# Kernel tuning notes

Hardware: AMD Instinct MI355X
Metric: run time of the kernel (lower is better)

Reference implementation:

```python
import jax, jax.numpy as jnp
import numpy as np

T, B, I, H, O = 2048, 128, 32, 128, 1


def setup_inputs() -> dict:
    key = jax.random.key(0)
    ks = jax.random.split(key, 5)
    X = jax.random.normal(ks[0], (T, B, I), dtype=jnp.float32)
    W_in = jax.random.normal(ks[1], (H, I), dtype=jnp.float32) / np.sqrt(I)
    W_hh = jax.random.normal(ks[2], (H, H), dtype=jnp.float32) / np.sqrt(H)
    rnn_bias = jnp.zeros((H,), dtype=jnp.float32)
    alpha = jax.random.uniform(ks[3], (H,), dtype=jnp.float32)
    value_W = jax.random.normal(ks[4], (O, H), dtype=jnp.float32) / np.sqrt(H)
    value_bias = jnp.zeros((O,), dtype=jnp.float32)
    return {"X": X, "W_in": W_in, "W_hh": W_hh, "rnn_bias": rnn_bias,
            "alpha": alpha, "value_W": value_W, "value_bias": value_bias}


def reference(X, W_in, W_hh, rnn_bias, alpha, value_W, value_bias):
    # X: (T, B, I). Precompute input projections for all timesteps at once.
    xproj = jnp.einsum('tbi,hi->tbh', X, W_in)  # (T, B, H)

    def step(h_prev, xp_t):
        h_tilde = jnp.tanh(xp_t + h_prev @ W_hh.T + rnn_bias)
        h = (1.0 - alpha) * h_prev + alpha * h_tilde  # per-unit leaky blend
        return h, h

    h0 = jnp.zeros((X.shape[1], W_hh.shape[0]), dtype=X.dtype)
    last_hidden, Z = jax.lax.scan(step, h0, xproj)  # Z: (T, B, H)
    V = value_bias + jnp.einsum('tbh,oh->tbo', Z, value_W)  # (T, B, O)
    return V, last_hidden
```

## Files before the change

kernel.cpp:

```cpp
#include <hip/hip_runtime.h>

#define TT 2048
#define BB 128
#define II 32
#define HH 128

typedef float v2f __attribute__((ext_vector_type(2)));
typedef float v4f __attribute__((ext_vector_type(4)));

__device__ __forceinline__ v2f pk_fma(v2f a, v2f b, v2f c) {
    v2f d;
    asm("v_pk_fma_f32 %0, %1, %2, %3" : "=v"(d) : "v"(a), "v"(b), "v"(c));
    return d;
}

template <int CTRL>
__device__ __forceinline__ float dpp_add(float p) {
    int t = __builtin_amdgcn_update_dpp(0, __float_as_int(p), CTRL, 0xF, 0xF, true);
    return p + __int_as_float(t);
}

__global__ __launch_bounds__(512)
void vrnn_kernel(const float* __restrict__ X, const float* __restrict__ W_in,
                 const float* __restrict__ W_hh, const float* __restrict__ rnn_bias,
                 const float* __restrict__ alpha, const float* __restrict__ value_W,
                 const float* __restrict__ value_bias, float* __restrict__ out)
{
    const int b    = blockIdx.x;
    const int tid  = threadIdx.x;
    const int wave = tid >> 6;
    const int lane = tid & 63;
    const int g    = lane >> 4;
    const int j    = lane & 15;
    const int base = 16 * wave + 4 * g;

    __shared__ __align__(16) float hbuf[2 * HH];
    __shared__ __align__(16) float xs[2 * 288];
    __shared__ __align__(16) float vpart[2][8];

    v2f wh[4][4], wi[4], binit[4];
#pragma unroll
    for (int r = 0; r < 4; ++r) {
        const float* wr = W_hh + (size_t)(base + r) * HH + 8 * j;
        v4f a0 = *reinterpret_cast<const v4f*>(wr);
        v4f a1 = *reinterpret_cast<const v4f*>(wr + 4);
        wh[r][0] = (v2f){a0.x, a0.y}; wh[r][1] = (v2f){a0.z, a0.w};
        wh[r][2] = (v2f){a1.x, a1.y}; wh[r][3] = (v2f){a1.z, a1.w};
        wi[r] = *reinterpret_cast<const v2f*>(W_in + (size_t)(base + r) * II + 2 * j);
        binit[r] = (v2f){ (j == 0) ? rnn_bias[base + r] : 0.0f, 0.0f };
    }
    const bool j1 = (j & 1) != 0;
    const bool j2 = (j & 2) != 0;
    const float al     = alpha[base + (j & 3)];
    const float vw_eff = (j < 4) ? value_W[base + j] : 0.0f;
    const float vb     = value_bias[0];

    if (tid < HH) hbuf[tid] = 0.0f;

    const int xr = lane >> 3;
    const int xc = (lane & 7) * 4;
    v4f xpend;
    if (wave == 0) {
        v4f w0 = *reinterpret_cast<const v4f*>(X + (size_t)xr * (BB * II) + b * II + xc);
        xpend  = *reinterpret_cast<const v4f*>(X + (size_t)(8 + xr) * (BB * II) + b * II + xc);
        *reinterpret_cast<v4f*>(&xs[xr * 36 + xc]) = w0;
    }
    float hval = 0.0f;
    __syncthreads();

    float* outV = out;
    float* outH = out + (size_t)TT * BB;

    for (int t2 = 0; t2 < TT / 16; ++t2) {
#pragma unroll
        for (int s = 0; s < 16; ++s) {
            if ((s & 7) == 0 && wave == 0) {
                *reinterpret_cast<v4f*>(&xs[(((s >> 3) + 1) & 1) * 288 + xr * 36 + xc]) = xpend;
                int row = (t2 << 4) + ((s >> 3) << 3) + 16 + xr;
                if (row > TT - 1) row = TT - 1;
                xpend = *reinterpret_cast<const v4f*>(X + (size_t)row * (BB * II) + b * II + xc);
            }
            if ((s != 0 || t2 != 0) && tid == 0) {
                const float* vp = vpart[(s & 1) ^ 1];
                float sum = vb;
#pragma unroll
                for (int w = 0; w < 8; ++w) sum += vp[w];
                const int t = (t2 << 4) + s;
                outV[(size_t)(t - 1) * BB + b] = sum;
            }
            const float* hb = &hbuf[(s & 1) * HH + 8 * j];
            v4f h0 = *reinterpret_cast<const v4f*>(hb);
            v4f h1 = *reinterpret_cast<const v4f*>(hb + 4);
            v2f hc0 = (v2f){h0.x, h0.y}, hc1 = (v2f){h0.z, h0.w};
            v2f hc2 = (v2f){h1.x, h1.y}, hc3 = (v2f){h1.z, h1.w};
            v2f xv = *reinterpret_cast<const v2f*>(&xs[((s >> 3) & 1) * 288 + (s & 7) * 36 + 2 * j]);
            float p0, p1, p2, p3;
            {
                v2f a;
                a = binit[0];
                a = pk_fma(wh[0][0], hc0, a); a = pk_fma(wh[0][1], hc1, a);
                a = pk_fma(wh[0][2], hc2, a); a = pk_fma(wh[0][3], hc3, a);
                a = pk_fma(wi[0], xv, a);
                p0 = a.x + a.y;
                a = binit[1];
                a = pk_fma(wh[1][0], hc0, a); a = pk_fma(wh[1][1], hc1, a);
                a = pk_fma(wh[1][2], hc2, a); a = pk_fma(wh[1][3], hc3, a);
                a = pk_fma(wi[1], xv, a);
                p1 = a.x + a.y;
                a = binit[2];
                a = pk_fma(wh[2][0], hc0, a); a = pk_fma(wh[2][1], hc1, a);
                a = pk_fma(wh[2][2], hc2, a); a = pk_fma(wh[2][3], hc3, a);
                a = pk_fma(wi[2], xv, a);
                p2 = a.x + a.y;
                a = binit[3];
                a = pk_fma(wh[3][0], hc0, a); a = pk_fma(wh[3][1], hc1, a);
                a = pk_fma(wh[3][2], hc2, a); a = pk_fma(wh[3][3], hc3, a);
                a = pk_fma(wi[3], xv, a);
                p3 = a.x + a.y;
            }
            p0 = dpp_add<0xB1>(p0); p0 = dpp_add<0x4E>(p0); p0 = dpp_add<0x124>(p0); p0 = dpp_add<0x128>(p0);
            p1 = dpp_add<0xB1>(p1); p1 = dpp_add<0x4E>(p1); p1 = dpp_add<0x124>(p1); p1 = dpp_add<0x128>(p1);
            p2 = dpp_add<0xB1>(p2); p2 = dpp_add<0x4E>(p2); p2 = dpp_add<0x124>(p2); p2 = dpp_add<0x128>(p2);
            p3 = dpp_add<0xB1>(p3); p3 = dpp_add<0x4E>(p3); p3 = dpp_add<0x124>(p3); p3 = dpp_add<0x128>(p3);
            const float sa  = j1 ? p1 : p0;
            const float sb  = j1 ? p3 : p2;
            const float pre = j2 ? sb : sa;
            const float e  = __builtin_amdgcn_exp2f(pre * 2.8853900817779268f);
            const float rc = __builtin_amdgcn_rcpf(e + 1.0f);
            const float ht = fmaf(-2.0f, rc, 1.0f);
            hval = fmaf(al, ht - hval, hval);
            if (j < 4) hbuf[((s & 1) ^ 1) * HH + base + j] = hval;
            float c = vw_eff * hval;
            c = dpp_add<0xB1>(c); c = dpp_add<0x4E>(c);
            const float c1 = __int_as_float(__builtin_amdgcn_readlane(__float_as_int(c), 16));
            const float c2 = __int_as_float(__builtin_amdgcn_readlane(__float_as_int(c), 32));
            const float c3 = __int_as_float(__builtin_amdgcn_readlane(__float_as_int(c), 48));
            if (lane == 0) vpart[s & 1][wave] = c + c1 + c2 + c3;
            asm volatile("s_waitcnt lgkmcnt(0)" ::: "memory");
            __builtin_amdgcn_s_barrier();
            __builtin_amdgcn_sched_barrier(0);
        }
    }
    if (tid == 0) {
        const float* vp = vpart[(TT - 1) & 1];
        float sum = vb;
#pragma unroll
        for (int w = 0; w < 8; ++w) sum += vp[w];
        outV[(size_t)(TT - 1) * BB + b] = sum;
    }
    if (j < 4) outH[b * HH + base + j] = hval;
}

extern "C" void kernel_launch(void* const* d_in, const int* in_sizes, int n_in,
                              void* d_out, int out_size, void* d_ws, size_t ws_size,
                              hipStream_t stream) {
    const float* X      = (const float*)d_in[0];
    const float* W_in   = (const float*)d_in[1];
    const float* W_hh   = (const float*)d_in[2];
    const float* rbias  = (const float*)d_in[3];
    const float* alpha  = (const float*)d_in[4];
    const float* vW     = (const float*)d_in[5];
    const float* vbias  = (const float*)d_in[6];
    float* out = (float*)d_out;

    vrnn_kernel<<<dim3(BB), dim3(512), 0, stream>>>(X, W_in, W_hh, rbias, alpha, vW, vbias, out);
}
```

Measured before the change: 755.6 us.

## Exchange tanh outputs instead of hidden state and split recurrence off critical path

Rewrites the recurrence algebraically: each thread keeps a full replicated copy of h and shares only the tanh output g through LDS. W_hh is split into W*alpha and W*(1-alpha), so the (1-alpha)h part of the matvec can be computed after the barrier, off the dependency chain. The value-head reduction becomes a per-wave DPP reduction written by a rotating wave, which removes the vpart LDS exchange. X loads now go straight to LDS via global_load_lds. The cost is more per-thread FMAs and registers, plus a change in rounding order.

```diff
diff --git a/kernel.cpp b/kernel.cpp
--- a/kernel.cpp
+++ b/kernel.cpp
@@ -4,9 +4,13 @@
 #define BB 128
 #define II 32
 #define HH 128
+#define NW (TT / 8)
 
 typedef float v2f __attribute__((ext_vector_type(2)));
 typedef float v4f __attribute__((ext_vector_type(4)));
+typedef unsigned int u32;
+typedef __attribute__((address_space(3))) u32 lds_u32;
+typedef const __attribute__((address_space(1))) u32 glb_u32;
 
 __device__ __forceinline__ v2f pk_fma(v2f a, v2f b, v2f c) {
     v2f d;
@@ -15,9 +19,12 @@
 }
 
 template <int CTRL>
+__device__ __forceinline__ float dpp_mov(float p) {
+    return __int_as_float(__builtin_amdgcn_update_dpp(0, __float_as_int(p), CTRL, 0xF, 0xF, true));
+}
+template <int CTRL>
 __device__ __forceinline__ float dpp_add(float p) {
-    int t = __builtin_amdgcn_update_dpp(0, __float_as_int(p), CTRL, 0xF, 0xF, true);
-    return p + __int_as_float(t);
+    return p + dpp_mov<CTRL>(p);
 }
 
 __global__ __launch_bounds__(512)
@@ -34,121 +41,145 @@
     const int j    = lane & 15;
     const int base = 16 * wave + 4 * g;
 
-    __shared__ __align__(16) float hbuf[2 * HH];
-    __shared__ __align__(16) float xs[2 * 288];
-    __shared__ __align__(16) float vpart[2][8];
+    __shared__ __align__(16) float xw[2][8][II];
+    __shared__ __align__(16) float gbuf[2][192];
 
-    v2f wh[4][4], wi[4], binit[4];
+    if (wave == 0) {
+        const float* src = X + (size_t)(lane >> 3) * (BB * II) + b * II + (lane & 7) * 4;
+        __builtin_amdgcn_global_load_lds((glb_u32*)src, (lds_u32*)(&xw[0][0][0]), 16, 0, 0);
+    }
+
+    v2f a_c[4], vwc[4];
+#pragma unroll
+    for (int i = 0; i < 4; ++i) {
+        a_c[i] = *(const v2f*)(alpha   + 8 * j + 2 * i);
+        vwc[i] = *(const v2f*)(value_W + 8 * j + 2 * i);
+    }
+    v2f m1[4][4], m2[4][4], wi[4], binit[4];
 #pragma unroll
     for (int r = 0; r < 4; ++r) {
         const float* wr = W_hh + (size_t)(base + r) * HH + 8 * j;
-        v4f a0 = *reinterpret_cast<const v4f*>(wr);
-        v4f a1 = *reinterpret_cast<const v4f*>(wr + 4);
-        wh[r][0] = (v2f){a0.x, a0.y}; wh[r][1] = (v2f){a0.z, a0.w};
-        wh[r][2] = (v2f){a1.x, a1.y}; wh[r][3] = (v2f){a1.z, a1.w};
-        wi[r] = *reinterpret_cast<const v2f*>(W_in + (size_t)(base + r) * II + 2 * j);
+#pragma unroll
+        for (int i = 0; i < 4; ++i) {
+            v2f w2 = *(const v2f*)(wr + 2 * i);
+            m2[r][i] = w2 * a_c[i];
+            m1[r][i] = w2 - m2[r][i];
+        }
+        wi[r]    = *(const v2f*)(W_in + (size_t)(base + r) * II + 2 * j);
         binit[r] = (v2f){ (j == 0) ? rnn_bias[base + r] : 0.0f, 0.0f };
     }
-    const bool j1 = (j & 1) != 0;
-    const bool j2 = (j & 2) != 0;
-    const float al     = alpha[base + (j & 3)];
-    const float vw_eff = (j < 4) ? value_W[base + j] : 0.0f;
-    const float vb     = value_bias[0];
+    const float vb = value_bias[0];
+    const int  hrow  = base + j;
+    const int  gwoff = 12 * (hrow >> 3) + (hrow & 7);
 
-    if (tid < HH) hbuf[tid] = 0.0f;
+    v2f hc[4], a1[4];
+#pragma unroll
+    for (int i = 0; i < 4; ++i) hc[i] = (v2f){0.f, 0.f};
+#pragma unroll
+    for (int r = 0; r < 4; ++r) a1[r] = binit[r];
 
-    const int xr = lane >> 3;
-    const int xc = (lane & 7) * 4;
-    v4f xpend;
-    if (wave == 0) {
-        v4f w0 = *reinterpret_cast<const v4f*>(X + (size_t)xr * (BB * II) + b * II + xc);
-        xpend  = *reinterpret_cast<const v4f*>(X + (size_t)(8 + xr) * (BB * II) + b * II + xc);
-        *reinterpret_cast<v4f*>(&xs[xr * 36 + xc]) = w0;
-    }
-    float hval = 0.0f;
+    if (tid < 192) gbuf[1][tid] = 0.0f;
     __syncthreads();
 
     float* outV = out;
     float* outH = out + (size_t)TT * BB;
 
-    for (int t2 = 0; t2 < TT / 16; ++t2) {
+    for (int w = 0; w < NW; ++w) {
+        if (wave == 0 && w + 1 < NW) {
+            const float* src = X + (size_t)((w + 1) * 8 + (lane >> 3)) * (BB * II)
+                                 + b * II + (lane & 7) * 4;
+            __builtin_amdgcn_global_load_lds((glb_u32*)src,
+                (lds_u32*)(&xw[(w + 1) & 1][0][0]), 16, 0, 0);
+        }
 #pragma unroll
-        for (int s = 0; s < 16; ++s) {
-            if ((s & 7) == 0 && wave == 0) {
-                *reinterpret_cast<v4f*>(&xs[(((s >> 3) + 1) & 1) * 288 + xr * 36 + xc]) = xpend;
-                int row = (t2 << 4) + ((s >> 3) << 3) + 16 + xr;
-                if (row > TT - 1) row = TT - 1;
-                xpend = *reinterpret_cast<const v4f*>(X + (size_t)row * (BB * II) + b * II + xc);
-            }
-            if ((s != 0 || t2 != 0) && tid == 0) {
-                const float* vp = vpart[(s & 1) ^ 1];
-                float sum = vb;
-#pragma unroll
-                for (int w = 0; w < 8; ++w) sum += vp[w];
-                const int t = (t2 << 4) + s;
-                outV[(size_t)(t - 1) * BB + b] = sum;
-            }
-            const float* hb = &hbuf[(s & 1) * HH + 8 * j];
-            v4f h0 = *reinterpret_cast<const v4f*>(hb);
-            v4f h1 = *reinterpret_cast<const v4f*>(hb + 4);
-            v2f hc0 = (v2f){h0.x, h0.y}, hc1 = (v2f){h0.z, h0.w};
-            v2f hc2 = (v2f){h1.x, h1.y}, hc3 = (v2f){h1.z, h1.w};
-            v2f xv = *reinterpret_cast<const v2f*>(&xs[((s >> 3) & 1) * 288 + (s & 7) * 36 + 2 * j]);
+        for (int s = 0; s < 8; ++s) {
+            const int par = s & 1;
+            const float* gb = &gbuf[par ^ 1][12 * j];
+            const v4f g0 = *(const v4f*)(gb);
+            const v4f g1 = *(const v4f*)(gb + 4);
+            v2f gp[4] = { (v2f){g0.x, g0.y}, (v2f){g0.z, g0.w},
+                          (v2f){g1.x, g1.y}, (v2f){g1.z, g1.w} };
+            const v2f xc = *(const v2f*)(&xw[w & 1][s][2 * j]);
             float p0, p1, p2, p3;
             {
                 v2f a;
-                a = binit[0];
-                a = pk_fma(wh[0][0], hc0, a); a = pk_fma(wh[0][1], hc1, a);
-                a = pk_fma(wh[0][2], hc2, a); a = pk_fma(wh[0][3], hc3, a);
-                a = pk_fma(wi[0], xv, a);
+                a = pk_fma(wi[0], xc, a1[0]);
+                a = pk_fma(m2[0][0], gp[0], a); a = pk_fma(m2[0][1], gp[1], a);
+                a = pk_fma(m2[0][2], gp[2], a); a = pk_fma(m2[0][3], gp[3], a);
                 p0 = a.x + a.y;
-                a = binit[1];
-                a = pk_fma(wh[1][0], hc0, a); a = pk_fma(wh[1][1], hc1, a);
-                a = pk_fma(wh[1][2], hc2, a); a = pk_fma(wh[1][3], hc3, a);
-                a = pk_fma(wi[1], xv, a);
+                a = pk_fma(wi[1], xc, a1[1]);
+                a = pk_fma(m2[1][0], gp[0], a); a = pk_fma(m2[1][1], gp[1], a);
+                a = pk_fma(m2[1][2], gp[2], a); a = pk_fma(m2[1][3], gp[3], a);
                 p1 = a.x + a.y;
-                a = binit[2];
-                a = pk_fma(wh[2][0], hc0, a); a = pk_fma(wh[2][1], hc1, a);
-                a = pk_fma(wh[2][2], hc2, a); a = pk_fma(wh[2][3], hc3, a);
-                a = pk_fma(wi[2], xv, a);
+                a = pk_fma(wi[2], xc, a1[2]);
+                a = pk_fma(m2[2][0], gp[0], a); a = pk_fma(m2[2][1], gp[1], a);
+                a = pk_fma(m2[2][2], gp[2], a); a = pk_fma(m2[2][3], gp[3], a);
                 p2 = a.x + a.y;
-                a = binit[3];
-                a = pk_fma(wh[3][0], hc0, a); a = pk_fma(wh[3][1], hc1, a);
-                a = pk_fma(wh[3][2], hc2, a); a = pk_fma(wh[3][3], hc3, a);
-                a = pk_fma(wi[3], xv, a);
+                a = pk_fma(wi[3], xc, a1[3]);
+                a = pk_fma(m2[3][0], gp[0], a); a = pk_fma(m2[3][1], gp[1], a);
+                a = pk_fma(m2[3][2], gp[2], a); a = pk_fma(m2[3][3], gp[3], a);
                 p3 = a.x + a.y;
             }
-            p0 = dpp_add<0xB1>(p0); p0 = dpp_add<0x4E>(p0); p0 = dpp_add<0x124>(p0); p0 = dpp_add<0x128>(p0);
-            p1 = dpp_add<0xB1>(p1); p1 = dpp_add<0x4E>(p1); p1 = dpp_add<0x124>(p1); p1 = dpp_add<0x128>(p1);
-            p2 = dpp_add<0xB1>(p2); p2 = dpp_add<0x4E>(p2); p2 = dpp_add<0x124>(p2); p2 = dpp_add<0x128>(p2);
-            p3 = dpp_add<0xB1>(p3); p3 = dpp_add<0x4E>(p3); p3 = dpp_add<0x124>(p3); p3 = dpp_add<0x128>(p3);
-            const float sa  = j1 ? p1 : p0;
-            const float sb  = j1 ? p3 : p2;
-            const float pre = j2 ? sb : sa;
+            const bool b0 = (j & 1) != 0;
+            const bool b1 = (j & 2) != 0;
+            float rA = (b0 ? p1 : p0) + dpp_mov<0xB1>(b0 ? p0 : p1);
+            float rB = (b0 ? p3 : p2) + dpp_mov<0xB1>(b0 ? p2 : p3);
+            float pre = (b1 ? rB : rA) + dpp_mov<0x4E>(b1 ? rA : rB);
+            pre = dpp_add<0x124>(pre);
+            pre = dpp_add<0x128>(pre);
             const float e  = __builtin_amdgcn_exp2f(pre * 2.8853900817779268f);
             const float rc = __builtin_amdgcn_rcpf(e + 1.0f);
-            const float ht = fmaf(-2.0f, rc, 1.0f);
-            hval = fmaf(al, ht - hval, hval);
-            if (j < 4) hbuf[((s & 1) ^ 1) * HH + base + j] = hval;
-            float c = vw_eff * hval;
-            c = dpp_add<0xB1>(c); c = dpp_add<0x4E>(c);
-            const float c1 = __int_as_float(__builtin_amdgcn_readlane(__float_as_int(c), 16));
-            const float c2 = __int_as_float(__builtin_amdgcn_readlane(__float_as_int(c), 32));
-            const float c3 = __int_as_float(__builtin_amdgcn_readlane(__float_as_int(c), 48));
-            if (lane == 0) vpart[s & 1][wave] = c + c1 + c2 + c3;
+            const float gt = fmaf(-2.0f, rc, 1.0f);
+            if (j < 4) gbuf[par][gwoff] = gt;
+#pragma unroll
+            for (int i = 0; i < 4; ++i) hc[i] = pk_fma(a_c[i], gp[i] - hc[i], hc[i]);
+            v2f vt = vwc[0] * hc[0];
+            vt = pk_fma(vwc[1], hc[1], vt);
+            vt = pk_fma(vwc[2], hc[2], vt);
+            vt = pk_fma(vwc[3], hc[3], vt);
+            float vsum = vt.x + vt.y;
+            vsum = dpp_add<0xB1>(vsum); vsum = dpp_add<0x4E>(vsum);
+            vsum = dpp_add<0x124>(vsum); vsum = dpp_add<0x128>(vsum);
+            if (wave == s && lane == 0 && (w + s) != 0)
+                outV[(size_t)(8 * w + s - 1) * BB + b] = vb + vsum;
+#pragma unroll
+            for (int r = 0; r < 4; ++r) {
+                v2f a = binit[r];
+                a = pk_fma(m1[r][0], hc[0], a); a = pk_fma(m1[r][1], hc[1], a);
+                a = pk_fma(m1[r][2], hc[2], a); a = pk_fma(m1[r][3], hc[3], a);
+                a1[r] = a;
+            }
+            if (wave == 0 && s == 7)
+                asm volatile("s_waitcnt vmcnt(0)" ::: "memory");
             asm volatile("s_waitcnt lgkmcnt(0)" ::: "memory");
             __builtin_amdgcn_s_barrier();
             __builtin_amdgcn_sched_barrier(0);
         }
     }
-    if (tid == 0) {
-        const float* vp = vpart[(TT - 1) & 1];
-        float sum = vb;
+
+    {
+        const float* gb = &gbuf[(TT - 1) & 1][12 * j];
+        const v4f g0 = *(const v4f*)(gb);
+        const v4f g1 = *(const v4f*)(gb + 4);
+        v2f gp[4] = { (v2f){g0.x, g0.y}, (v2f){g0.z, g0.w},
+                      (v2f){g1.x, g1.y}, (v2f){g1.z, g1.w} };
 #pragma unroll
-        for (int w = 0; w < 8; ++w) sum += vp[w];
-        outV[(size_t)(TT - 1) * BB + b] = sum;
+        for (int i = 0; i < 4; ++i) hc[i] = pk_fma(a_c[i], gp[i] - hc[i], hc[i]);
+        v2f vt = vwc[0] * hc[0];
+        vt = pk_fma(vwc[1], hc[1], vt);
+        vt = pk_fma(vwc[2], hc[2], vt);
+        vt = pk_fma(vwc[3], hc[3], vt);
+        float vsum = vt.x + vt.y;
+        vsum = dpp_add<0xB1>(vsum); vsum = dpp_add<0x4E>(vsum);
+        vsum = dpp_add<0x124>(vsum); vsum = dpp_add<0x128>(vsum);
+        if (wave == 0 && lane == 0)
+            outV[(size_t)(TT - 1) * BB + b] = vb + vsum;
+        if (wave == 0 && g == 0) {
+#pragma unroll
+            for (int i = 0; i < 4; ++i)
+                *(v2f*)(outH + (size_t)b * HH + 8 * j + 2 * i) = hc[i];
+        }
     }
-    if (j < 4) outH[b * HH + base + j] = hval;
 }
 
 extern "C" void kernel_launch(void* const* d_in, const int* in_sizes, int n_in,
```

Result: slower. 871.0 us (+15.3%).
